# Kernel tuning notes

Hardware: AMD Instinct MI355X
Metric: run time of the kernel (lower is better)

Reference implementation:

```python
import jax, jax.numpy as jnp
import numpy as np

N_USERS = 100000
N_ITEMS = 50000
N_NODES = N_USERS + N_ITEMS
DIM = 128
N_HOPS = 3
N_EDGES = 4800000


def setup_inputs() -> dict:
    key = jax.random.key(0)
    ks = jax.random.split(key, 7)
    user_embed = jax.random.normal(ks[0], (N_USERS, DIM), dtype=jnp.float32)
    item_embed = jax.random.normal(ks[1], (N_ITEMS, DIM), dtype=jnp.float32)
    # user_t / item_t are sigmoid(log(deg+e)) priors in (0,1)
    user_t = jax.random.uniform(ks[2], (N_USERS, 1), dtype=jnp.float32)
    item_t = jax.random.uniform(ks[3], (N_ITEMS, 1), dtype=jnp.float32)
    adj_vals = jax.random.uniform(ks[4], (N_EDGES,), dtype=jnp.float32)
    adj_rows = jax.random.randint(ks[5], (N_EDGES,), 0, N_NODES, dtype=jnp.int32)
    adj_cols = jax.random.randint(ks[6], (N_EDGES,), 0, N_NODES, dtype=jnp.int32)
    return {
        "user_embed": user_embed,
        "item_embed": item_embed,
        "user_t": user_t,
        "item_t": item_t,
        "adj_vals": adj_vals,
        "adj_rows": adj_rows,
        "adj_cols": adj_cols,
    }


def _spmm(vals, rows, cols, x):
    # y[r] += vals * x[cols]  -- sparse (N,N) @ dense (N,D)
    msgs = vals[:, None] * x[cols]
    return jax.ops.segment_sum(msgs, rows, num_segments=N_NODES)


def reference(user_embed, item_embed, user_t, item_t, adj_vals, adj_rows, adj_cols):
    # eval-mode GraphConv.forward (no edge/mess dropout)
    agg = jnp.concatenate([user_embed, item_embed], axis=0)  # [N, D]
    ego = jnp.concatenate([user_t * user_embed, item_t * item_embed], axis=0)
    embs = [ego]
    decay_u = 1.0 - user_t
    decay_i = 1.0 - item_t
    pow_u = jnp.ones_like(user_t)
    pow_i = jnp.ones_like(item_t)
    for _ in range(N_HOPS):
        side = _spmm(adj_vals, adj_rows, adj_cols, agg)  # [N, D]
        u_side, i_side = side[:N_USERS], side[N_USERS:]
        pow_u = pow_u * decay_u
        pow_i = pow_i * decay_i
        u_k = u_side * (user_t * pow_u)
        i_k = i_side * (item_t * pow_i)
        embs.append(jnp.concatenate([u_k, i_k], axis=0))
        agg = side
    embs = jnp.stack(embs, axis=1)  # [N, n_hops+1, D]
    return embs[:N_USERS], embs[N_USERS:]
```

## Files before the change

kernel.cpp:

```cpp
#include <hip/hip_runtime.h>

#define NU 100000
#define NI 50000
#define NN 150000
#define DIM 128
#define NHOPS 3
#define STR ((NHOPS + 1) * DIM)


__global__ void hist_kernel(const int* __restrict__ rows, int* deg, int E) {
  int i = blockIdx.x * blockDim.x + threadIdx.x;
  int stride = gridDim.x * blockDim.x;
  for (; i < E; i += stride) atomicAdd(&deg[rows[i]], 1);
}

__global__ void scan_k1(const int* __restrict__ deg, int* bsum, int n) {
  __shared__ int red[256];
  int b = blockIdx.x, t = threadIdx.x;
  int base = b * 2048 + t * 8;
  int s = 0;
#pragma unroll
  for (int j = 0; j < 8; ++j) { int i = base + j; if (i < n) s += deg[i]; }
  red[t] = s;
  __syncthreads();
  for (int off = 128; off > 0; off >>= 1) {
    if (t < off) red[t] += red[t + off];
    __syncthreads();
  }
  if (t == 0) bsum[b] = red[0];
}

__global__ void scan_k2(int* bsum, int nb) {
  if (threadIdx.x == 0) {
    int run = 0;
    for (int i = 0; i < nb; ++i) { int v = bsum[i]; bsum[i] = run; run += v; }
  }
}

__global__ void scan_k3(const int* __restrict__ deg, const int* __restrict__ bsum,
                        int* __restrict__ rstart, int* __restrict__ cursor, int n, int E) {
  __shared__ int red[256];
  int b = blockIdx.x, t = threadIdx.x;
  int base = b * 2048 + t * 8;
  int loc[8];
  int s = 0;
#pragma unroll
  for (int j = 0; j < 8; ++j) {
    int i = base + j;
    int d = (i < n) ? deg[i] : 0;
    loc[j] = s; s += d;
  }
  red[t] = s;
  __syncthreads();
  for (int off = 1; off < 256; off <<= 1) {
    int v = (t >= off) ? red[t - off] : 0;
    __syncthreads();
    red[t] += v;
    __syncthreads();
  }
  int toff = bsum[b] + red[t] - s;
#pragma unroll
  for (int j = 0; j < 8; ++j) {
    int i = base + j;
    if (i < n) { int v = toff + loc[j]; rstart[i] = v; cursor[i] = v; }
  }
  if (b == 0 && t == 0) rstart[n] = E;
}

__global__ void scatter_kernel(const int* __restrict__ rows, const int* __restrict__ cols,
                               const float* __restrict__ vals, int* cursor,
                               int2* __restrict__ csr, int E) {
  int i = blockIdx.x * blockDim.x + threadIdx.x;
  int stride = gridDim.x * blockDim.x;
  for (; i < E; i += stride) {
    int r = rows[i];
    int p = atomicAdd(&cursor[r], 1);
    int2 e; e.x = cols[i]; e.y = __float_as_int(vals[i]);
    csr[p] = e;
  }
}


__global__ void copy_embed_fused(const float* __restrict__ ue, const float* __restrict__ ie,
                                 const float* __restrict__ ut, const float* __restrict__ it,
                                 float* __restrict__ rawA, float* __restrict__ out) {
  int idx = blockIdx.x * blockDim.x + threadIdx.x;
  if (idx >= NN * (DIM / 4)) return;
  int node = idx >> 5;
  int d4 = idx & 31;
  float t;
  float4 x;
  if (node < NU) { t = ut[node]; x = ((const float4*)(ue + (size_t)node * DIM))[d4]; }
  else { t = it[node - NU]; x = ((const float4*)(ie + (size_t)(node - NU) * DIM))[d4]; }
  ((float4*)(rawA + (size_t)node * DIM))[d4] = x;
  float4 y; y.x = x.x * t; y.y = x.y * t; y.z = x.z * t; y.w = x.w * t;
  ((float4*)(out + (size_t)node * STR))[d4] = y;
}

__global__ void copy_embed_raw(const float* __restrict__ ue, const float* __restrict__ ie,
                               float* __restrict__ out) {
  int idx = blockIdx.x * blockDim.x + threadIdx.x;
  if (idx >= NN * (DIM / 4)) return;
  int node = idx >> 5;
  int d4 = idx & 31;
  const float4* src = (node < NU)
      ? ((const float4*)(ue + (size_t)node * DIM) + d4)
      : ((const float4*)(ie + (size_t)(node - NU) * DIM) + d4);
  ((float4*)(out + (size_t)node * STR))[d4] = *src;
}

__global__ __launch_bounds__(256) void spmm_kernel(
    const int* __restrict__ row_start, const int2* __restrict__ csr,
    const float* __restrict__ src, int src_str,
    float* raw_out, int raw_str,
    float* scaled_out, int scaled_str,
    const float* __restrict__ ut, const float* __restrict__ it, int hop) {
  int wave = (blockIdx.x * blockDim.x + threadIdx.x) >> 6;
  if (wave >= NN / 2) return;
  int lane = threadIdx.x & 63;
  int half = lane >> 5;
  int lane_in = lane & 31;
  int row = wave * 2 + half;
  int s = row_start[row];
  int e = row_start[row + 1];
  float ax = 0.f, ay = 0.f, az = 0.f, aw = 0.f;
  const float* src_base = src + lane_in * 4;
  int p = s;
  for (; p + 8 <= e; p += 8) {
    int2 ed = csr[p + (lane_in & 7)];
#pragma unroll
    for (int j = 0; j < 8; ++j) {
      int cc = __shfl(ed.x, j, 32);
      float vv = __int_as_float(__shfl(ed.y, j, 32));
      float4 x = *(const float4*)(src_base + (size_t)cc * src_str);
      ax += vv * x.x; ay += vv * x.y; az += vv * x.z; aw += vv * x.w;
    }
  }
  for (; p < e; ++p) {
    int2 ed = csr[p];
    float4 x = *(const float4*)(src_base + (size_t)ed.x * src_str);
    float vv = __int_as_float(ed.y);
    ax += vv * x.x; ay += vv * x.y; az += vv * x.z; aw += vv * x.w;
  }
  if (raw_out) {
    float4 o; o.x = ax; o.y = ay; o.z = az; o.w = aw;
    *(float4*)(raw_out + (size_t)row * raw_str + lane_in * 4) = o;
  }
  if (scaled_out) {
    float t = (row < NU) ? ut[row] : it[row - NU];
    float sc = t;
    for (int j = 0; j < hop; ++j) sc *= (1.f - t);
    float4 o; o.x = ax * sc; o.y = ay * sc; o.z = az * sc; o.w = aw * sc;
    *(float4*)(scaled_out + (size_t)row * scaled_str + lane_in * 4) = o;
  }
}

__global__ void epilogue_kernel(const float* __restrict__ ut, const float* __restrict__ it,
                                float* __restrict__ out) {
  int idx = blockIdx.x * blockDim.x + threadIdx.x;
  if (idx >= NN * 96) return;
  int node = idx / 96;
  int rem = idx - node * 96;
  int k = rem >> 5;
  int d4 = rem & 31;
  float t = (node < NU) ? ut[node] : it[node - NU];
  float dcy = 1.f - t;
  float sc = t;
  for (int j = 0; j < k; ++j) sc *= dcy;
  float4* p = (float4*)(out + (size_t)node * STR + k * DIM) + d4;
  float4 x = *p;
  x.x *= sc; x.y *= sc; x.z *= sc; x.w *= sc;
  *p = x;
}


extern "C" void kernel_launch(void* const* d_in, const int* in_sizes, int n_in,
                              void* d_out, int out_size, void* d_ws, size_t ws_size,
                              hipStream_t stream) {
  const float* ue = (const float*)d_in[0];
  const float* ie = (const float*)d_in[1];
  const float* ut = (const float*)d_in[2];
  const float* it = (const float*)d_in[3];
  const float* vals = (const float*)d_in[4];
  const int* rows = (const int*)d_in[5];
  const int* cols = (const int*)d_in[6];
  float* out = (float*)d_out;
  const int E = in_sizes[4];

  size_t off = 0;
  auto alloc = [&](size_t bytes) {
    void* p = (char*)d_ws + off;
    off += (bytes + 255) & ~(size_t)255;
    return p;
  };
  int* deg = (int*)alloc((size_t)NN * 4);
  int* cursor = (int*)alloc((size_t)NN * 4);
  int* rstart = (int*)alloc(((size_t)NN + 1) * 4);
  int* bsum = (int*)alloc(1024 * 4);
  int2* csr = (int2*)alloc((size_t)E * 8);
  size_t csr_end = off;
  float* rawA = (float*)alloc((size_t)NN * DIM * 4);
  float* rawB = (float*)alloc((size_t)NN * DIM * 4);
  bool use_csr = (csr_end <= ws_size);
  bool use_compact = (off <= ws_size);

  const int n4_embed = NN * (DIM / 4);
  const int nb_scan = (NN + 2047) / 2048;
  const int spmm_blocks = (NN / 2 + 3) / 4;

  if (use_csr) {
    hipMemsetAsync(deg, 0, (size_t)NN * 4, stream);
    hist_kernel<<<2048, 256, 0, stream>>>(rows, deg, E);
    scan_k1<<<nb_scan, 256, 0, stream>>>(deg, bsum, NN);
    scan_k2<<<1, 64, 0, stream>>>(bsum, nb_scan);
    scan_k3<<<nb_scan, 256, 0, stream>>>(deg, bsum, rstart, cursor, NN, E);
    scatter_kernel<<<2048, 256, 0, stream>>>(rows, cols, vals, cursor, csr, E);

    if (use_compact) {
      copy_embed_fused<<<(n4_embed + 255) / 256, 256, 0, stream>>>(ue, ie, ut, it, rawA, out);
      float* rin = rawA;
      float* rout = rawB;
      for (int h = 1; h <= NHOPS; ++h) {
        float* raw_dst = (h < NHOPS) ? rout : nullptr;
        spmm_kernel<<<spmm_blocks, 256, 0, stream>>>(rstart, csr, rin, DIM,
                                                     raw_dst, DIM,
                                                     out + h * DIM, STR, ut, it, h);
        float* tmp = rin; rin = rout; rout = tmp;
      }
    } else {
      copy_embed_raw<<<(n4_embed + 255) / 256, 256, 0, stream>>>(ue, ie, out);
      for (int h = 1; h <= NHOPS; ++h) {
        float* raw_dst = (h < NHOPS) ? (out + h * DIM) : nullptr;
        float* sc_dst = (h == NHOPS) ? (out + h * DIM) : nullptr;
        spmm_kernel<<<spmm_blocks, 256, 0, stream>>>(rstart, csr, out + (h - 1) * DIM, STR,
                                                     raw_dst, STR, sc_dst, STR, ut, it, h);
      }
      epilogue_kernel<<<(NN * 96 + 255) / 256, 256, 0, stream>>>(ut, it, out);
    }
  }
}
```

Before: 1.965 ms.

## Build CSR via two-level bucket partition instead of global atomic scatter

Replaces the direct atomic histogram and scatter into CSR with a two-pass radix-style partition. Edges are first binned into 128-row buckets using shared-memory histograms and sub-binned cursors. Per-bucket degree and CSR placement then run with localized atomics, and the rawA buffer is reused as temporary storage. The goal is to cut contention from scattered global atomics and random writes during CSR construction, at the cost of extra kernel launches and an extra pass over the edge data.

```diff
diff --git a/kernel.cpp b/kernel.cpp
--- a/kernel.cpp
+++ b/kernel.cpp
@@ -7,11 +7,29 @@
 #define NHOPS 3
 #define STR ((NHOPS + 1) * DIM)
 
+#define NBK 1172
+#define NSUB 8
+#define NBINS (NBK * NSUB)
+#define PART_GRID 1024
+
 
 __global__ void hist_kernel(const int* __restrict__ rows, int* deg, int E) {
   int i = blockIdx.x * blockDim.x + threadIdx.x;
   int stride = gridDim.x * blockDim.x;
   for (; i < E; i += stride) atomicAdd(&deg[rows[i]], 1);
+}
+
+__global__ void scatter_kernel(const int* __restrict__ rows, const int* __restrict__ cols,
+                               const float* __restrict__ vals, int* cursor,
+                               int2* __restrict__ csr, int E) {
+  int i = blockIdx.x * blockDim.x + threadIdx.x;
+  int stride = gridDim.x * blockDim.x;
+  for (; i < E; i += stride) {
+    int r = rows[i];
+    int p = atomicAdd(&cursor[r], 1);
+    int2 e; e.x = cols[i]; e.y = __float_as_int(vals[i]);
+    csr[p] = e;
+  }
 }
 
 __global__ void scan_k1(const int* __restrict__ deg, int* bsum, int n) {
@@ -67,16 +85,65 @@
   if (b == 0 && t == 0) rstart[n] = E;
 }
 
-__global__ void scatter_kernel(const int* __restrict__ rows, const int* __restrict__ cols,
-                               const float* __restrict__ vals, int* cursor,
-                               int2* __restrict__ csr, int E) {
+
+__global__ void bucket_hist(const int* __restrict__ rows, int* bdeg, int E) {
+  __shared__ int h[NBK];
+  for (int j = threadIdx.x; j < NBK; j += blockDim.x) h[j] = 0;
+  __syncthreads();
+  int i = blockIdx.x * blockDim.x + threadIdx.x;
+  int stride = gridDim.x * blockDim.x;
+  for (; i < E; i += stride) atomicAdd(&h[rows[i] >> 7], 1);
+  __syncthreads();
+  int sub = blockIdx.x & (NSUB - 1);
+  for (int j = threadIdx.x; j < NBK; j += blockDim.x) {
+    int v = h[j];
+    if (v) atomicAdd(&bdeg[j * NSUB + sub], v);
+  }
+}
+
+__global__ void bucket_scatter(const int* __restrict__ rows, const int* __restrict__ cols,
+                               const float* __restrict__ vals, int* bcursor,
+                               int* __restrict__ brow, int2* __restrict__ bcv, int E) {
+  int sub = blockIdx.x & (NSUB - 1);
   int i = blockIdx.x * blockDim.x + threadIdx.x;
   int stride = gridDim.x * blockDim.x;
   for (; i < E; i += stride) {
     int r = rows[i];
+    int p = atomicAdd(&bcursor[(r >> 7) * NSUB + sub], 1);
+    brow[p] = r;
+    int2 e2; e2.x = cols[i]; e2.y = __float_as_int(vals[i]);
+    bcv[p] = e2;
+  }
+}
+
+__global__ void deg_from_buckets(const int* __restrict__ boff, const int* __restrict__ brow,
+                                 int* __restrict__ deg) {
+  __shared__ int h[128];
+  int b = blockIdx.x;
+  if (threadIdx.x < 128) h[threadIdx.x] = 0;
+  __syncthreads();
+  int base = b * 128;
+  int s = boff[b * NSUB];
+  int e = boff[b * NSUB + NSUB];
+  for (int i = s + threadIdx.x; i < e; i += blockDim.x)
+    atomicAdd(&h[brow[i] - base], 1);
+  __syncthreads();
+  if (threadIdx.x < 128) {
+    int r = base + threadIdx.x;
+    if (r < NN) deg[r] = h[threadIdx.x];
+  }
+}
+
+__global__ void csr_from_buckets(const int* __restrict__ boff, const int* __restrict__ brow,
+                                 const int2* __restrict__ bcv, int* cursor,
+                                 int2* __restrict__ csr) {
+  int b = blockIdx.x;
+  int s = boff[b * NSUB];
+  int e = boff[b * NSUB + NSUB];
+  for (int i = s + threadIdx.x; i < e; i += blockDim.x) {
+    int r = brow[i];
     int p = atomicAdd(&cursor[r], 1);
-    int2 e; e.x = cols[i]; e.y = __float_as_int(vals[i]);
-    csr[p] = e;
+    csr[p] = bcv[i];
   }
 }
 
@@ -197,6 +264,9 @@
   int* cursor = (int*)alloc((size_t)NN * 4);
   int* rstart = (int*)alloc(((size_t)NN + 1) * 4);
   int* bsum = (int*)alloc(1024 * 4);
+  int* bdeg = (int*)alloc((size_t)NBINS * 4);
+  int* boff = (int*)alloc(((size_t)NBINS + 1) * 4);
+  int* bcursor = (int*)alloc((size_t)NBINS * 4);
   int2* csr = (int2*)alloc((size_t)E * 8);
   size_t csr_end = off;
   float* rawA = (float*)alloc((size_t)NN * DIM * 4);
@@ -204,19 +274,28 @@
   bool use_csr = (csr_end <= ws_size);
   bool use_compact = (off <= ws_size);
 
+  int* brow = (int*)rawA;
+  int2* bcv = (int2*)((char*)rawA + ((size_t)E * 4 + 255 & ~(size_t)255));
+
   const int n4_embed = NN * (DIM / 4);
   const int nb_scan = (NN + 2047) / 2048;
+  const int nb_scan_b = (NBINS + 2047) / 2048;
   const int spmm_blocks = (NN / 2 + 3) / 4;
 
   if (use_csr) {
-    hipMemsetAsync(deg, 0, (size_t)NN * 4, stream);
-    hist_kernel<<<2048, 256, 0, stream>>>(rows, deg, E);
-    scan_k1<<<nb_scan, 256, 0, stream>>>(deg, bsum, NN);
-    scan_k2<<<1, 64, 0, stream>>>(bsum, nb_scan);
-    scan_k3<<<nb_scan, 256, 0, stream>>>(deg, bsum, rstart, cursor, NN, E);
-    scatter_kernel<<<2048, 256, 0, stream>>>(rows, cols, vals, cursor, csr, E);
-
     if (use_compact) {
+      hipMemsetAsync(bdeg, 0, (size_t)NBINS * 4, stream);
+      bucket_hist<<<PART_GRID, 256, 0, stream>>>(rows, bdeg, E);
+      scan_k1<<<nb_scan_b, 256, 0, stream>>>(bdeg, bsum, NBINS);
+      scan_k2<<<1, 64, 0, stream>>>(bsum, nb_scan_b);
+      scan_k3<<<nb_scan_b, 256, 0, stream>>>(bdeg, bsum, boff, bcursor, NBINS, E);
+      bucket_scatter<<<PART_GRID, 256, 0, stream>>>(rows, cols, vals, bcursor, brow, bcv, E);
+      deg_from_buckets<<<NBK, 256, 0, stream>>>(boff, brow, deg);
+      scan_k1<<<nb_scan, 256, 0, stream>>>(deg, bsum, NN);
+      scan_k2<<<1, 64, 0, stream>>>(bsum, nb_scan);
+      scan_k3<<<nb_scan, 256, 0, stream>>>(deg, bsum, rstart, cursor, NN, E);
+      csr_from_buckets<<<NBK, 256, 0, stream>>>(boff, brow, bcv, cursor, csr);
+
       copy_embed_fused<<<(n4_embed + 255) / 256, 256, 0, stream>>>(ue, ie, ut, it, rawA, out);
       float* rin = rawA;
       float* rout = rawB;
@@ -228,6 +307,13 @@
         float* tmp = rin; rin = rout; rout = tmp;
       }
     } else {
+      hipMemsetAsync(deg, 0, (size_t)NN * 4, stream);
+      hist_kernel<<<2048, 256, 0, stream>>>(rows, deg, E);
+      scan_k1<<<nb_scan, 256, 0, stream>>>(deg, bsum, NN);
+      scan_k2<<<1, 64, 0, stream>>>(bsum, nb_scan);
+      scan_k3<<<nb_scan, 256, 0, stream>>>(deg, bsum, rstart, cursor, NN, E);
+      scatter_kernel<<<2048, 256, 0, stream>>>(rows, cols, vals, cursor, csr, E);
+
       copy_embed_raw<<<(n4_embed + 255) / 256, 256, 0, stream>>>(ue, ie, out);
       for (int h = 1; h <= NHOPS; ++h) {
         float* raw_dst = (h < NHOPS) ? (out + h * DIM) : nullptr;
```

Result: faster. 1.885 ms (-4.1%).
